# Kernel optimization log

Measured on AMD Instinct MI355X. Metric: run time of the kernel, lower is better.

## Reference

```python
import jax, jax.numpy as jnp
import numpy as np

N_NODES = 50000
N_EDGES = 800000
F_IN = 128
HID = 128
N_CLASSES = 16
N_GRAPHS = 64


def _glorot(key, shape):
    fan_in, fan_out = shape[0], shape[1]
    lim = (6.0 / (fan_in + fan_out)) ** 0.5
    return jax.random.uniform(key, shape, jnp.float32, -lim, lim)


def setup_inputs() -> dict:
    key = jax.random.key(0)
    ks = jax.random.split(key, 12)
    x = jax.random.normal(ks[0], (N_NODES, F_IN), jnp.float32)
    edge_index = jax.random.randint(ks[1], (2, N_EDGES), 0, N_NODES, jnp.int64)
    batch = jnp.sort(jax.random.randint(ks[2], (N_NODES,), 0, N_GRAPHS, jnp.int64))
    W0 = _glorot(ks[3], (F_IN, HID)); b0 = jnp.zeros((HID,), jnp.float32)
    W1 = _glorot(ks[4], (HID, HID)); b1 = jnp.zeros((HID,), jnp.float32)
    W2 = _glorot(ks[5], (HID, HID)); b2 = jnp.zeros((HID,), jnp.float32)
    Wc = _glorot(ks[6], (HID, N_CLASSES)); bc = jnp.zeros((N_CLASSES,), jnp.float32)
    return {"x": x, "edge_index": edge_index, "batch": batch,
            "W0": W0, "b0": b0, "W1": W1, "b1": b1, "W2": W2, "b2": b2,
            "Wc": Wc, "bc": bc}


def _gcn_prep(edge_index, n_nodes):
    # add self-loops, compute symmetric normalization coefficients
    loop = jnp.arange(n_nodes, dtype=edge_index.dtype)
    src = jnp.concatenate([edge_index[0], loop])
    dst = jnp.concatenate([edge_index[1], loop])
    deg = jax.ops.segment_sum(jnp.ones_like(dst, jnp.float32), dst, num_segments=n_nodes)
    dinv = deg ** -0.5  # deg >= 1 due to self-loops
    norm = dinv[src] * dinv[dst]  # [E+N]
    return src, dst, norm


def _gcn_layer(h, W, b, src, dst, norm, n_nodes):
    h = h @ W                                   # [N, out]
    msg = h[src] * norm[:, None]                # gather + scale [E+N, out]
    out = jax.ops.segment_sum(msg, dst, num_segments=n_nodes)  # scatter-add
    return out + b


def reference(x, edge_index, batch, W0, b0, W1, b1, W2, b2, Wc, bc):
    n = x.shape[0]
    src, dst, norm = _gcn_prep(edge_index, n)
    h = _gcn_layer(x, W0, b0, src, dst, norm, n)
    h = jax.nn.relu(h)  # dropout is identity in eval mode
    h = _gcn_layer(h, W1, b1, src, dst, norm, n)
    h = jax.nn.relu(h)
    h = _gcn_layer(h, W2, b2, src, dst, norm, n)
    # scatter-mean pooling over batch ids
    sums = jax.ops.segment_sum(h, batch, num_segments=N_GRAPHS)        # [G, HID]
    cnts = jax.ops.segment_sum(jnp.ones((n,), jnp.float32), batch, num_segments=N_GRAPHS)
    pooled = sums / jnp.maximum(cnts, 1.0)[:, None]
    return pooled @ Wc + bc  # [G, N_CLASSES]
```

## Files before the change

kernel.cpp:

```cpp
#include <hip/hip_runtime.h>
#include <hip/hip_bf16.h>
#include <hip/hip_fp16.h>

#define HID 128
#define NCLS 16
#define NGRAPH 64
#define CHUNK 1024

using bf16x8 = __attribute__((ext_vector_type(8))) short;
using f32x4  = __attribute__((ext_vector_type(4))) float;

__device__ __forceinline__ unsigned int f2bf(float f) {
    unsigned int u = __float_as_uint(f);
    return (u + 0x7FFFu + ((u >> 16) & 1u)) >> 16;
}
__device__ __forceinline__ float bf2f_lo(unsigned int u) { return __uint_as_float(u << 16); }
__device__ __forceinline__ float bf2f_hi(unsigned int u) { return __uint_as_float(u & 0xFFFF0000u); }

__global__ __launch_bounds__(256) void k_init(int* counts, float* pooled, float* cnt, int n) {
    int i = blockIdx.x * 256 + threadIdx.x;
    if (i < n) counts[i] = 0;
    if (i < NGRAPH * HID) pooled[i] = 0.0f;
    if (i < NGRAPH) cnt[i] = 0.0f;
}

__global__ __launch_bounds__(256) void k_hist(const int* __restrict__ dst,
                                              int* counts, int* rank, int e) {
    int i = blockIdx.x * 256 + threadIdx.x;
    if (i < e) rank[i] = atomicAdd(&counts[dst[i]], 1);
}

__global__ __launch_bounds__(256) void k_dinv(const int* __restrict__ counts,
                                              float* dinv, int n) {
    int i = blockIdx.x * 256 + threadIdx.x;
    if (i < n) dinv[i] = rsqrtf((float)(counts[i] + 1));
}

__global__ __launch_bounds__(256) void k_chunksum(const int* __restrict__ counts,
                                                  int* csum, int n) {
    __shared__ int sdata[256];
    int b = blockIdx.x, t = threadIdx.x;
    int base = b * CHUNK + t * 4;
    int s = 0;
    #pragma unroll
    for (int j = 0; j < 4; ++j) { int i = base + j; if (i < n) s += counts[i]; }
    sdata[t] = s; __syncthreads();
    for (int off = 128; off > 0; off >>= 1) {
        if (t < off) sdata[t] += sdata[t + off];
        __syncthreads();
    }
    if (t == 0) csum[b] = sdata[0];
}

__global__ void k_scanchunks(const int* __restrict__ csum, int* coff, int nb) {
    if (blockIdx.x == 0 && threadIdx.x == 0) {
        int run = 0;
        for (int b = 0; b < nb; ++b) { coff[b] = run; run += csum[b]; }
    }
}

__global__ __launch_bounds__(256) void k_rowptr(const int* __restrict__ counts,
                                                const int* __restrict__ coff,
                                                int* rowptr, int n, int e) {
    __shared__ int sincl[256];
    int b = blockIdx.x, t = threadIdx.x;
    int base = b * CHUNK + t * 4;
    int v[4]; int s = 0;
    #pragma unroll
    for (int j = 0; j < 4; ++j) { int i = base + j; v[j] = (i < n) ? counts[i] : 0; s += v[j]; }
    sincl[t] = s; __syncthreads();
    for (int off = 1; off < 256; off <<= 1) {
        int x = sincl[t];
        int y = (t >= off) ? sincl[t - off] : 0;
        __syncthreads();
        sincl[t] = x + y;
        __syncthreads();
    }
    int run = coff[b] + sincl[t] - s;
    #pragma unroll
    for (int j = 0; j < 4; ++j) {
        int i = base + j;
        if (i < n) { rowptr[i] = run; run += v[j]; }
    }
    if (b == 0 && t == 0) rowptr[n] = e;
}

__global__ __launch_bounds__(256) void k_fill(const int* __restrict__ src,
                                              const int* __restrict__ dst,
                                              const int* __restrict__ rank,
                                              const float* __restrict__ dinv,
                                              const int* __restrict__ rowptr,
                                              unsigned int* __restrict__ epk, int e) {
    int i = blockIdx.x * 256 + threadIdx.x;
    if (i >= e) return;
    int s = src[i], d = dst[i];
    int pos = rowptr[d] + rank[i];
    __half h = __float2half(dinv[s] * dinv[d]);
    unsigned int hu = (unsigned int)__half_as_ushort(h);
    epk[pos] = (unsigned int)s | (hu << 16);
}

__global__ __launch_bounds__(256) void k_wprep(const float* __restrict__ W0,
                                               const float* __restrict__ W1,
                                               const float* __restrict__ W2,
                                               unsigned short* __restrict__ Wt) {
    int tid = blockIdx.x * 256 + threadIdx.x;
    if (tid >= 3 * HID * HID) return;
    int m = tid >> 14;
    int r = tid & 16383;
    int c = r >> 7, k = r & 127;
    const float* W = (m == 0) ? W0 : (m == 1) ? W1 : W2;
    Wt[tid] = (unsigned short)f2bf(W[k * HID + c]);
}

__global__ __launch_bounds__(256) void k_gemm(const float* __restrict__ H,
                                              const unsigned short* __restrict__ Wt,
                                              unsigned short* __restrict__ Tb16,
                                              int n, int relu_in) {
    __shared__ char ldsA[64 * 256];
    int t = threadIdx.x;
    int cg = t & 31;
    int rg = t >> 5;
    int row0 = blockIdx.x * 64;

    #pragma unroll
    for (int i = 0; i < 8; ++i) {
        int lr = rg + i * 8;
        int r = row0 + lr;
        float4 v = make_float4(0.f, 0.f, 0.f, 0.f);
        if (r < n) v = ((const float4*)H)[(size_t)r * 32 + cg];
        if (relu_in) {
            v.x = fmaxf(v.x, 0.f); v.y = fmaxf(v.y, 0.f);
            v.z = fmaxf(v.z, 0.f); v.w = fmaxf(v.w, 0.f);
        }
        uint2 pk;
        pk.x = f2bf(v.x) | (f2bf(v.y) << 16);
        pk.y = f2bf(v.z) | (f2bf(v.w) << 16);
        int byte = lr * 256 + cg * 8;
        *(uint2*)(ldsA + (byte ^ ((lr & 7) << 4))) = pk;
    }
    __syncthreads();

    int lane = t & 63;
    int w = t >> 6;
    int rsub = lane & 15;
    int kg = lane >> 4;
    int rowIdx = w * 16 + rsub;
    int abase = rowIdx * 256 + kg * 16;
    int aswz = (rowIdx & 7) << 4;

    f32x4 acc[8];
    #pragma unroll
    for (int nt = 0; nt < 8; ++nt) acc[nt] = (f32x4)(0.f);

    #pragma unroll
    for (int kk = 0; kk < 4; ++kk) {
        bf16x8 a = *(const bf16x8*)(ldsA + ((abase + kk * 64) ^ aswz));
        int k0 = kk * 32 + kg * 8;
        #pragma unroll
        for (int nt = 0; nt < 8; ++nt) {
            int col = nt * 16 + rsub;
            bf16x8 b = *(const bf16x8*)(Wt + col * 128 + k0);
            acc[nt] = __builtin_amdgcn_mfma_f32_16x16x32_bf16(a, b, acc[nt], 0, 0, 0);
        }
    }

    #pragma unroll
    for (int nt = 0; nt < 8; ++nt) {
        #pragma unroll
        for (int j = 0; j < 4; ++j) {
            int row = row0 + w * 16 + kg * 4 + j;
            int col = nt * 16 + rsub;
            if (row < n) Tb16[(size_t)row * 128 + col] = (unsigned short)f2bf(acc[nt][j]);
        }
    }
}

__global__ __launch_bounds__(256) void k_agg(const unsigned int* __restrict__ Tb,
                                             float* __restrict__ O,
                                             const int* __restrict__ rowptr,
                                             const unsigned int* __restrict__ epk,
                                             const float* __restrict__ dinv,
                                             const float* __restrict__ bias, int n) {
    int wid = (blockIdx.x * 256 + threadIdx.x) >> 6;
    int lane = threadIdx.x & 63;
    if (wid >= n) return;
    float di = dinv[wid];
    float2 b2 = ((const float2*)bias)[lane];
    unsigned int us = Tb[(size_t)wid * 64 + lane];
    float sn = di * di;
    float2 acc;
    acc.x = fmaf(bf2f_lo(us), sn, b2.x);
    acc.y = fmaf(bf2f_hi(us), sn, b2.y);
    int start = rowptr[wid];
    int deg = rowptr[wid + 1] - start;

    for (int j0 = 0; j0 < deg; j0 += 64) {
        int myj = j0 + lane;
        unsigned int rec = 0;
        if (myj < deg) rec = epk[start + myj];
        int m = min(64, deg - j0);
        int jj = 0;
        for (; jj + 8 <= m; jj += 8) {
            int r0 = __shfl((int)rec, jj + 0), r1 = __shfl((int)rec, jj + 1);
            int r2 = __shfl((int)rec, jj + 2), r3 = __shfl((int)rec, jj + 3);
            int r4 = __shfl((int)rec, jj + 4), r5 = __shfl((int)rec, jj + 5);
            int r6 = __shfl((int)rec, jj + 6), r7 = __shfl((int)rec, jj + 7);
            unsigned int u0 = Tb[(size_t)(r0 & 0xFFFF) * 64 + lane];
            unsigned int u1 = Tb[(size_t)(r1 & 0xFFFF) * 64 + lane];
            unsigned int u2 = Tb[(size_t)(r2 & 0xFFFF) * 64 + lane];
            unsigned int u3 = Tb[(size_t)(r3 & 0xFFFF) * 64 + lane];
            unsigned int u4 = Tb[(size_t)(r4 & 0xFFFF) * 64 + lane];
            unsigned int u5 = Tb[(size_t)(r5 & 0xFFFF) * 64 + lane];
            unsigned int u6 = Tb[(size_t)(r6 & 0xFFFF) * 64 + lane];
            unsigned int u7 = Tb[(size_t)(r7 & 0xFFFF) * 64 + lane];
            float w0 = __half2float(__ushort_as_half((unsigned short)((unsigned)r0 >> 16)));
            float w1 = __half2float(__ushort_as_half((unsigned short)((unsigned)r1 >> 16)));
            float w2 = __half2float(__ushort_as_half((unsigned short)((unsigned)r2 >> 16)));
            float w3 = __half2float(__ushort_as_half((unsigned short)((unsigned)r3 >> 16)));
            float w4 = __half2float(__ushort_as_half((unsigned short)((unsigned)r4 >> 16)));
            float w5 = __half2float(__ushort_as_half((unsigned short)((unsigned)r5 >> 16)));
            float w6 = __half2float(__ushort_as_half((unsigned short)((unsigned)r6 >> 16)));
            float w7 = __half2float(__ushort_as_half((unsigned short)((unsigned)r7 >> 16)));
            acc.x = fmaf(w0, bf2f_lo(u0), acc.x); acc.y = fmaf(w0, bf2f_hi(u0), acc.y);
            acc.x = fmaf(w1, bf2f_lo(u1), acc.x); acc.y = fmaf(w1, bf2f_hi(u1), acc.y);
            acc.x = fmaf(w2, bf2f_lo(u2), acc.x); acc.y = fmaf(w2, bf2f_hi(u2), acc.y);
            acc.x = fmaf(w3, bf2f_lo(u3), acc.x); acc.y = fmaf(w3, bf2f_hi(u3), acc.y);
            acc.x = fmaf(w4, bf2f_lo(u4), acc.x); acc.y = fmaf(w4, bf2f_hi(u4), acc.y);
            acc.x = fmaf(w5, bf2f_lo(u5), acc.x); acc.y = fmaf(w5, bf2f_hi(u5), acc.y);
            acc.x = fmaf(w6, bf2f_lo(u6), acc.x); acc.y = fmaf(w6, bf2f_hi(u6), acc.y);
            acc.x = fmaf(w7, bf2f_lo(u7), acc.x); acc.y = fmaf(w7, bf2f_hi(u7), acc.y);
        }
        for (; jj < m; ++jj) {
            int rj = __shfl((int)rec, jj);
            unsigned int u = Tb[(size_t)(rj & 0xFFFF) * 64 + lane];
            float wj = __half2float(__ushort_as_half((unsigned short)((unsigned)rj >> 16)));
            acc.x = fmaf(wj, bf2f_lo(u), acc.x);
            acc.y = fmaf(wj, bf2f_hi(u), acc.y);
        }
    }
    ((float2*)O)[(size_t)wid * 64 + lane] = acc;
}

__global__ __launch_bounds__(256) void k_pool(const float* __restrict__ H,
                                              const int* __restrict__ batch,
                                              float* pooled, float* cnt, int n) {
    int gw = (blockIdx.x * 256 + threadIdx.x) >> 6;
    int lane = threadIdx.x & 63;
    int n0 = gw * 32;
    if (n0 >= n) return;
    int n1 = min(n0 + 32, n);
    const float2* H2 = (const float2*)H;
    int gprev = batch[n0];
    float2 acc = make_float2(0.f, 0.f);
    float runc = 0.f;
    for (int i = n0; i < n1; ++i) {
        int g = batch[i];
        if (g != gprev) {
            atomicAdd(&pooled[gprev * HID + 2 * lane], acc.x);
            atomicAdd(&pooled[gprev * HID + 2 * lane + 1], acc.y);
            if (lane == 0) atomicAdd(&cnt[gprev], runc);
            acc = make_float2(0.f, 0.f); runc = 0.f; gprev = g;
        }
        float2 v = H2[(size_t)i * 64 + lane];
        acc.x += v.x; acc.y += v.y; runc += 1.f;
    }
    atomicAdd(&pooled[gprev * HID + 2 * lane], acc.x);
    atomicAdd(&pooled[gprev * HID + 2 * lane + 1], acc.y);
    if (lane == 0) atomicAdd(&cnt[gprev], runc);
}

__global__ __launch_bounds__(256) void k_head(const float* __restrict__ pooled,
                                              const float* __restrict__ cnt,
                                              const float* __restrict__ Wc,
                                              const float* __restrict__ bc,
                                              float* __restrict__ out) {
    int idx = blockIdx.x * 256 + threadIdx.x;
    if (idx >= NGRAPH * NCLS) return;
    int g = idx >> 4, c = idx & 15;
    float inv = 1.0f / fmaxf(cnt[g], 1.0f);
    float s = 0.f;
    for (int k = 0; k < HID; ++k)
        s = fmaf(pooled[g * HID + k], Wc[k * NCLS + c], s);
    out[idx] = s * inv + bc[c];
}

extern "C" void kernel_launch(void* const* d_in, const int* in_sizes, int n_in,
                              void* d_out, int out_size, void* d_ws, size_t ws_size,
                              hipStream_t stream) {
    const float* x    = (const float*)d_in[0];
    const int*   ei   = (const int*)d_in[1];
    const int*   batch= (const int*)d_in[2];
    const float* W0   = (const float*)d_in[3];
    const float* b0   = (const float*)d_in[4];
    const float* W1   = (const float*)d_in[5];
    const float* b1   = (const float*)d_in[6];
    const float* W2   = (const float*)d_in[7];
    const float* b2   = (const float*)d_in[8];
    const float* Wc   = (const float*)d_in[9];
    const float* bc   = (const float*)d_in[10];
    float* out = (float*)d_out;

    const int N = in_sizes[0] / HID;
    const int E = in_sizes[1] / 2;
    const int* src = ei;
    const int* dst = ei + E;

    char* p = (char*)d_ws;
    auto alloc = [&](size_t bytes) { void* r = (void*)p; p += (bytes + 255) & ~(size_t)255; return r; };
    int*   counts = (int*)alloc((size_t)N * 4);
    float* dinv   = (float*)alloc((size_t)N * 4);
    int*   rank   = (int*)alloc((size_t)E * 4);
    int*   csum   = (int*)alloc(256 * 4);
    int*   coff   = (int*)alloc(256 * 4);
    int*   rowptr = (int*)alloc((size_t)(N + 1) * 4);
    unsigned int* epk = (unsigned int*)alloc((size_t)E * 4);
    float* pooled = (float*)alloc((size_t)NGRAPH * HID * 4);
    float* cnt    = (float*)alloc((size_t)NGRAPH * 4);
    unsigned short* Tb16 = (unsigned short*)alloc((size_t)N * HID * 2);
    float* bufF   = (float*)alloc((size_t)N * HID * 4);
    unsigned short* Wt = (unsigned short*)alloc((size_t)3 * HID * HID * 2);

    const int NB = (N + CHUNK - 1) / CHUNK;

    k_init<<<(N + 255) / 256, 256, 0, stream>>>(counts, pooled, cnt, N);
    k_hist<<<(E + 255) / 256, 256, 0, stream>>>(dst, counts, rank, E);
    k_dinv<<<(N + 255) / 256, 256, 0, stream>>>(counts, dinv, N);
    k_chunksum<<<NB, 256, 0, stream>>>(counts, csum, N);
    k_scanchunks<<<1, 64, 0, stream>>>(csum, coff, NB);
    k_rowptr<<<NB, 256, 0, stream>>>(counts, coff, rowptr, N, E);
    k_fill<<<(E + 255) / 256, 256, 0, stream>>>(src, dst, rank, dinv, rowptr, epk, E);
    k_wprep<<<(3 * HID * HID + 255) / 256, 256, 0, stream>>>(W0, W1, W2, Wt);

    const int gemm_grid = (N + 63) / 64;
    const int agg_grid  = ((size_t)N * 64 + 255) / 256;

    k_gemm<<<gemm_grid, 256, 0, stream>>>(x, Wt, Tb16, N, 0);
    k_agg<<<agg_grid, 256, 0, stream>>>((const unsigned int*)Tb16, bufF, rowptr, epk, dinv, b0, N);
    k_gemm<<<gemm_grid, 256, 0, stream>>>(bufF, Wt + 16384, Tb16, N, 1);
    k_agg<<<agg_grid, 256, 0, stream>>>((const unsigned int*)Tb16, bufF, rowptr, epk, dinv, b1, N);
    k_gemm<<<gemm_grid, 256, 0, stream>>>(bufF, Wt + 32768, Tb16, N, 1);
    k_agg<<<agg_grid, 256, 0, stream>>>((const unsigned int*)Tb16, bufF, rowptr, epk, dinv, b2, N);

    const int pool_waves = (N + 31) / 32;
    k_pool<<<(pool_waves * 64 + 255) / 256, 256, 0, stream>>>(bufF, batch, pooled, cnt, N);
    k_head<<<(NGRAPH * NCLS + 255) / 256, 256, 0, stream>>>(pooled, cnt, Wc, bc, out);
}
```

Measured before the change: 268.0 us.

## Fuse ReLU and bf16 packing into aggregation output; add bf16-input GEMM

The aggregation kernel now applies ReLU and writes bf16 hidden activations for the first two layers, and a new GEMM reads those bf16 rows straight into LDS without fp32 loads or conversion. This halves the intermediate write and read traffic between aggregation and GEMM. The gather loop is also restructured into 16-wide and 4-wide unrolled batches to keep more loads in flight. Numerics are unchanged because the GEMM already rounded its input to bf16.

```diff
diff --git a/kernel.cpp b/kernel.cpp
--- a/kernel.cpp
+++ b/kernel.cpp
@@ -113,10 +113,9 @@
     Wt[tid] = (unsigned short)f2bf(W[k * HID + c]);
 }
 
-__global__ __launch_bounds__(256) void k_gemm(const float* __restrict__ H,
-                                              const unsigned short* __restrict__ Wt,
-                                              unsigned short* __restrict__ Tb16,
-                                              int n, int relu_in) {
+__global__ __launch_bounds__(256) void k_gemm_f32(const float* __restrict__ H,
+                                                  const unsigned short* __restrict__ Wt,
+                                                  unsigned short* __restrict__ Tb16, int n) {
     __shared__ char ldsA[64 * 256];
     int t = threadIdx.x;
     int cg = t & 31;
@@ -129,10 +128,6 @@
         int r = row0 + lr;
         float4 v = make_float4(0.f, 0.f, 0.f, 0.f);
         if (r < n) v = ((const float4*)H)[(size_t)r * 32 + cg];
-        if (relu_in) {
-            v.x = fmaxf(v.x, 0.f); v.y = fmaxf(v.y, 0.f);
-            v.z = fmaxf(v.z, 0.f); v.w = fmaxf(v.w, 0.f);
-        }
         uint2 pk;
         pk.x = f2bf(v.x) | (f2bf(v.y) << 16);
         pk.y = f2bf(v.z) | (f2bf(v.w) << 16);
@@ -176,12 +171,69 @@
     }
 }
 
+__global__ __launch_bounds__(256) void k_gemm_bf16(const unsigned short* __restrict__ Hb,
+                                                   const unsigned short* __restrict__ Wt,
+                                                   unsigned short* __restrict__ Tb16, int n) {
+    __shared__ char ldsA[64 * 256];
+    int t = threadIdx.x;
+    int row0 = blockIdx.x * 64;
+    int c16 = t & 15;
+    int rbase = t >> 4;
+
+    #pragma unroll
+    for (int i = 0; i < 4; ++i) {
+        int lr = rbase + i * 16;
+        int r = row0 + lr;
+        uint4 v = make_uint4(0u, 0u, 0u, 0u);
+        if (r < n) v = *(const uint4*)(Hb + (size_t)r * 128 + c16 * 8);
+        int byte = lr * 256 + c16 * 16;
+        *(uint4*)(ldsA + (byte ^ ((lr & 7) << 4))) = v;
+    }
+    __syncthreads();
+
+    int lane = t & 63;
+    int w = t >> 6;
+    int rsub = lane & 15;
+    int kg = lane >> 4;
+    int rowIdx = w * 16 + rsub;
+    int abase = rowIdx * 256 + kg * 16;
+    int aswz = (rowIdx & 7) << 4;
+
+    f32x4 acc[8];
+    #pragma unroll
+    for (int nt = 0; nt < 8; ++nt) acc[nt] = (f32x4)(0.f);
+
+    #pragma unroll
+    for (int kk = 0; kk < 4; ++kk) {
+        bf16x8 a = *(const bf16x8*)(ldsA + ((abase + kk * 64) ^ aswz));
+        int k0 = kk * 32 + kg * 8;
+        #pragma unroll
+        for (int nt = 0; nt < 8; ++nt) {
+            int col = nt * 16 + rsub;
+            bf16x8 b = *(const bf16x8*)(Wt + col * 128 + k0);
+            acc[nt] = __builtin_amdgcn_mfma_f32_16x16x32_bf16(a, b, acc[nt], 0, 0, 0);
+        }
+    }
+
+    #pragma unroll
+    for (int nt = 0; nt < 8; ++nt) {
+        #pragma unroll
+        for (int j = 0; j < 4; ++j) {
+            int row = row0 + w * 16 + kg * 4 + j;
+            int col = nt * 16 + rsub;
+            if (row < n) Tb16[(size_t)row * 128 + col] = (unsigned short)f2bf(acc[nt][j]);
+        }
+    }
+}
+
 __global__ __launch_bounds__(256) void k_agg(const unsigned int* __restrict__ Tb,
-                                             float* __restrict__ O,
+                                             unsigned int* __restrict__ outB,
+                                             float* __restrict__ outF,
                                              const int* __restrict__ rowptr,
                                              const unsigned int* __restrict__ epk,
                                              const float* __restrict__ dinv,
-                                             const float* __restrict__ bias, int n) {
+                                             const float* __restrict__ bias,
+                                             int n, int mode) {
     int wid = (blockIdx.x * 256 + threadIdx.x) >> 6;
     int lane = threadIdx.x & 63;
     if (wid >= n) return;
@@ -201,45 +253,47 @@
         if (myj < deg) rec = epk[start + myj];
         int m = min(64, deg - j0);
         int jj = 0;
-        for (; jj + 8 <= m; jj += 8) {
-            int r0 = __shfl((int)rec, jj + 0), r1 = __shfl((int)rec, jj + 1);
-            int r2 = __shfl((int)rec, jj + 2), r3 = __shfl((int)rec, jj + 3);
-            int r4 = __shfl((int)rec, jj + 4), r5 = __shfl((int)rec, jj + 5);
-            int r6 = __shfl((int)rec, jj + 6), r7 = __shfl((int)rec, jj + 7);
-            unsigned int u0 = Tb[(size_t)(r0 & 0xFFFF) * 64 + lane];
-            unsigned int u1 = Tb[(size_t)(r1 & 0xFFFF) * 64 + lane];
-            unsigned int u2 = Tb[(size_t)(r2 & 0xFFFF) * 64 + lane];
-            unsigned int u3 = Tb[(size_t)(r3 & 0xFFFF) * 64 + lane];
-            unsigned int u4 = Tb[(size_t)(r4 & 0xFFFF) * 64 + lane];
-            unsigned int u5 = Tb[(size_t)(r5 & 0xFFFF) * 64 + lane];
-            unsigned int u6 = Tb[(size_t)(r6 & 0xFFFF) * 64 + lane];
-            unsigned int u7 = Tb[(size_t)(r7 & 0xFFFF) * 64 + lane];
-            float w0 = __half2float(__ushort_as_half((unsigned short)((unsigned)r0 >> 16)));
-            float w1 = __half2float(__ushort_as_half((unsigned short)((unsigned)r1 >> 16)));
-            float w2 = __half2float(__ushort_as_half((unsigned short)((unsigned)r2 >> 16)));
-            float w3 = __half2float(__ushort_as_half((unsigned short)((unsigned)r3 >> 16)));
-            float w4 = __half2float(__ushort_as_half((unsigned short)((unsigned)r4 >> 16)));
-            float w5 = __half2float(__ushort_as_half((unsigned short)((unsigned)r5 >> 16)));
-            float w6 = __half2float(__ushort_as_half((unsigned short)((unsigned)r6 >> 16)));
-            float w7 = __half2float(__ushort_as_half((unsigned short)((unsigned)r7 >> 16)));
-            acc.x = fmaf(w0, bf2f_lo(u0), acc.x); acc.y = fmaf(w0, bf2f_hi(u0), acc.y);
-            acc.x = fmaf(w1, bf2f_lo(u1), acc.x); acc.y = fmaf(w1, bf2f_hi(u1), acc.y);
-            acc.x = fmaf(w2, bf2f_lo(u2), acc.x); acc.y = fmaf(w2, bf2f_hi(u2), acc.y);
-            acc.x = fmaf(w3, bf2f_lo(u3), acc.x); acc.y = fmaf(w3, bf2f_hi(u3), acc.y);
-            acc.x = fmaf(w4, bf2f_lo(u4), acc.x); acc.y = fmaf(w4, bf2f_hi(u4), acc.y);
-            acc.x = fmaf(w5, bf2f_lo(u5), acc.x); acc.y = fmaf(w5, bf2f_hi(u5), acc.y);
-            acc.x = fmaf(w6, bf2f_lo(u6), acc.x); acc.y = fmaf(w6, bf2f_hi(u6), acc.y);
-            acc.x = fmaf(w7, bf2f_lo(u7), acc.x); acc.y = fmaf(w7, bf2f_hi(u7), acc.y);
+        for (; jj + 16 <= m; jj += 16) {
+            unsigned int rr[16], uu[16];
+            #pragma unroll
+            for (int k = 0; k < 16; ++k) rr[k] = (unsigned int)__shfl((int)rec, jj + k);
+            #pragma unroll
+            for (int k = 0; k < 16; ++k) uu[k] = Tb[(size_t)(rr[k] & 0xFFFFu) * 64 + lane];
+            #pragma unroll
+            for (int k = 0; k < 16; ++k) {
+                float wk = __half2float(__ushort_as_half((unsigned short)(rr[k] >> 16)));
+                acc.x = fmaf(wk, bf2f_lo(uu[k]), acc.x);
+                acc.y = fmaf(wk, bf2f_hi(uu[k]), acc.y);
+            }
+        }
+        for (; jj + 4 <= m; jj += 4) {
+            unsigned int rr[4], uu[4];
+            #pragma unroll
+            for (int k = 0; k < 4; ++k) rr[k] = (unsigned int)__shfl((int)rec, jj + k);
+            #pragma unroll
+            for (int k = 0; k < 4; ++k) uu[k] = Tb[(size_t)(rr[k] & 0xFFFFu) * 64 + lane];
+            #pragma unroll
+            for (int k = 0; k < 4; ++k) {
+                float wk = __half2float(__ushort_as_half((unsigned short)(rr[k] >> 16)));
+                acc.x = fmaf(wk, bf2f_lo(uu[k]), acc.x);
+                acc.y = fmaf(wk, bf2f_hi(uu[k]), acc.y);
+            }
         }
         for (; jj < m; ++jj) {
-            int rj = __shfl((int)rec, jj);
-            unsigned int u = Tb[(size_t)(rj & 0xFFFF) * 64 + lane];
-            float wj = __half2float(__ushort_as_half((unsigned short)((unsigned)rj >> 16)));
+            unsigned int rj = (unsigned int)__shfl((int)rec, jj);
+            unsigned int u = Tb[(size_t)(rj & 0xFFFFu) * 64 + lane];
+            float wj = __half2float(__ushort_as_half((unsigned short)(rj >> 16)));
             acc.x = fmaf(wj, bf2f_lo(u), acc.x);
             acc.y = fmaf(wj, bf2f_hi(u), acc.y);
         }
     }
-    ((float2*)O)[(size_t)wid * 64 + lane] = acc;
+
+    if (mode == 0) {
+        float rx = fmaxf(acc.x, 0.f), ry = fmaxf(acc.y, 0.f);
+        outB[(size_t)wid * 64 + lane] = f2bf(rx) | (f2bf(ry) << 16);
+    } else {
+        ((float2*)outF)[(size_t)wid * 64 + lane] = acc;
+    }
 }
 
 __global__ __launch_bounds__(256) void k_pool(const float* __restrict__ H,
@@ -318,6 +372,7 @@
     float* pooled = (float*)alloc((size_t)NGRAPH * HID * 4);
     float* cnt    = (float*)alloc((size_t)NGRAPH * 4);
     unsigned short* Tb16 = (unsigned short*)alloc((size_t)N * HID * 2);
+    unsigned short* Hb16 = (unsigned short*)alloc((size_t)N * HID * 2);
     float* bufF   = (float*)alloc((size_t)N * HID * 4);
     unsigned short* Wt = (unsigned short*)alloc((size_t)3 * HID * HID * 2);
 
@@ -335,12 +390,15 @@
     const int gemm_grid = (N + 63) / 64;
     const int agg_grid  = ((size_t)N * 64 + 255) / 256;
 
-    k_gemm<<<gemm_grid, 256, 0, stream>>>(x, Wt, Tb16, N, 0);
-    k_agg<<<agg_grid, 256, 0, stream>>>((const unsigned int*)Tb16, bufF, rowptr, epk, dinv, b0, N);
-    k_gemm<<<gemm_grid, 256, 0, stream>>>(bufF, Wt + 16384, Tb16, N, 1);
-    k_agg<<<agg_grid, 256, 0, stream>>>((const unsigned int*)Tb16, bufF, rowptr, epk, dinv, b1, N);
-    k_gemm<<<gemm_grid, 256, 0, stream>>>(bufF, Wt + 32768, Tb16, N, 1);
-    k_agg<<<agg_grid, 256, 0, stream>>>((const unsigned int*)Tb16, bufF, rowptr, epk, dinv, b2, N);
+    k_gemm_f32<<<gemm_grid, 256, 0, stream>>>(x, Wt, Tb16, N);
+    k_agg<<<agg_grid, 256, 0, stream>>>((const unsigned int*)Tb16, (unsigned int*)Hb16, nullptr,
+                                        rowptr, epk, dinv, b0, N, 0);
+    k_gemm_bf16<<<gemm_grid, 256, 0, stream>>>(Hb16, Wt + 16384, Tb16, N);
+    k_agg<<<agg_grid, 256, 0, stream>>>((const unsigned int*)Tb16, (unsigned int*)Hb16, nullptr,
+                                        rowptr, epk, dinv, b1, N, 0);
+    k_gemm_bf16<<<gemm_grid, 256, 0, stream>>>(Hb16, Wt + 32768, Tb16, N);
+    k_agg<<<agg_grid, 256, 0, stream>>>((const unsigned int*)Tb16, nullptr, bufF,
+                                        rowptr, epk, dinv, b2, N, 1);
 
     const int pool_waves = (N + 31) / 32;
     k_pool<<<(pool_waves * 64 + 255) / 256, 256, 0, stream>>>(bufF, batch, pooled, cnt, N);
```

After: 264.5 us. No clear change (-1.3%).
